# Kernel optimization log

Hardware: AMD Instinct MI355X
Metric: run time of the kernel (lower is better)

The kernel has to match this reference:

```python
import jax, jax.numpy as jnp
import numpy as np

B, S, IN, OUT, SPLIT = 4, 2048, 4096, 4096, 1024


def setup_inputs() -> dict:
    key = jax.random.key(0)
    ks = jax.random.split(key, 14)
    def n(k, shape, scale=1.0):
        return jax.random.normal(k, shape, dtype=jnp.float32) * scale
    return {
        "x": n(ks[0], (B, S, IN)),
        "V": n(ks[1], (SPLIT, IN)),
        "U": n(ks[2], (OUT, SPLIT)),
        "v2": n(ks[3], (1, IN), 0.05),
        "v1": n(ks[4], (1, SPLIT), 0.05),
        "u2": n(ks[5], (1, SPLIT), 0.05),
        "u1": n(ks[6], (1, OUT), 0.05),
        "V_R": n(ks[7], (SPLIT, IN)),
        "U_R": n(ks[8], (OUT, SPLIT)),
        "v2_R": n(ks[9], (1, IN), 0.05),
        "v1_R": n(ks[10], (1, SPLIT), 0.05),
        "u2_R": n(ks[11], (1, SPLIT), 0.05),
        "u1_R": n(ks[12], (1, OUT), 0.05),
        "bias": n(ks[13], (OUT,), 0.02),
    }


def _quantize(w):
    # ITQ binarization: sign(w) with straight-through estimator semantics
    return w + jax.lax.stop_gradient(jnp.sign(w) - w)


def _compute_forward(x2d, V, U, v2, v1, u2, u1):
    # x2d: [T, in]; V: [split, in]; U: [out, split]
    Vq = _quantize(V)
    Uq = _quantize(U)
    v1u2 = v1 * u2  # [1, split]
    h = (x2d * v2) @ Vq.T          # [T, split]
    return (h * v1u2) @ Uq.T * u1  # [T, out]


def reference(x, V, U, v2, v1, u2, u1, V_R, U_R, v2_R, v1_R, u2_R, u1_R, bias):
    lead = x.shape[:-1]
    x2d = x.reshape(-1, x.shape[-1])
    y = _compute_forward(x2d, V, U, v2, v1, u2, u1)
    y = y + _compute_forward(x2d, V_R, U_R, v2_R, v1_R, u2_R, u1_R)
    y = y + bias
    return y.reshape(lead + (U.shape[0],))
```

## Files before the change

### kernel.cpp

```cpp
#include <hip/hip_runtime.h>


typedef __bf16 bf16x8 __attribute__((ext_vector_type(8)));
typedef float floatx4 __attribute__((ext_vector_type(4)));

__device__ __forceinline__ unsigned short f2bf_rne(float f) {
    union { float f; unsigned u; } v; v.f = f;
    unsigned r = v.u + 0x7FFFu + ((v.u >> 16) & 1u);
    return (unsigned short)(r >> 16);
}

__device__ __forceinline__ float sgnf(float w) {
    return (float)((w > 0.f) - (w < 0.f));
}

__device__ __forceinline__ void async_copy16(const void* g, void* l) {
    __builtin_amdgcn_global_load_lds(
        (const __attribute__((address_space(1))) void*)g,
        (__attribute__((address_space(3))) void*)l, 16, 0, 0);
}

#define FENCE() asm volatile("" ::: "memory")
#define BAR() do { FENCE(); __builtin_amdgcn_s_barrier(); FENCE(); } while (0)
#define VMW(N) asm volatile("s_waitcnt vmcnt(" #N ")" ::: "memory")
#define LGKM(N) asm volatile("s_waitcnt lgkmcnt(" #N ")" ::: "memory")


__global__ void prep_all_kernel(const float* __restrict__ x,
                                unsigned short* __restrict__ xb,
                                const float* __restrict__ V, const float* __restrict__ V_R,
                                const float* __restrict__ v2, const float* __restrict__ v2_R,
                                const float* __restrict__ U, const float* __restrict__ U_R,
                                const float* __restrict__ v1, const float* __restrict__ v1_R,
                                const float* __restrict__ u2, const float* __restrict__ u2_R,
                                const float* __restrict__ u1, const float* __restrict__ u1_R,
                                unsigned short* __restrict__ W1,
                                unsigned short* __restrict__ W2) {
    int bid = blockIdx.x;
    if (bid < 32768) {
        int i = bid * blockDim.x + threadIdx.x;
        float4 v = ((const float4*)x)[i];
        ushort4 o;
        o.x = f2bf_rne(v.x); o.y = f2bf_rne(v.y);
        o.z = f2bf_rne(v.z); o.w = f2bf_rne(v.w);
        ((ushort4*)xb)[i] = o;
    } else if (bid < 40960) {
        int i = (bid - 32768) * blockDim.x + threadIdx.x;
        int idx = i << 2;
        int scat = idx >> 12;
        int k = idx & 4095;
        const float* Vp; const float* sp;
        if (scat < 1024) { Vp = V + ((size_t)scat << 12); sp = v2; }
        else             { Vp = V_R + ((size_t)(scat - 1024) << 12); sp = v2_R; }
        float4 w = *(const float4*)(Vp + k);
        float4 s = *(const float4*)(sp + k);
        ushort4 o;
        o.x = f2bf_rne(sgnf(w.x) * s.x);
        o.y = f2bf_rne(sgnf(w.y) * s.y);
        o.z = f2bf_rne(sgnf(w.z) * s.z);
        o.w = f2bf_rne(sgnf(w.w) * s.w);
        ((ushort4*)W1)[i] = o;
    } else {
        int i = (bid - 40960) * blockDim.x + threadIdx.x;
        int idx = i << 2;
        int o = idx >> 11;
        int scat = idx & 2047;
        int branch = scat >> 10;
        int s = scat & 1023;
        const float* Up  = branch ? U_R  : U;
        const float* v1p = branch ? v1_R : v1;
        const float* u2p = branch ? u2_R : u2;
        float u1v = (branch ? u1_R : u1)[o];
        float4 w = *(const float4*)(Up + ((size_t)o << 10) + s);
        float4 a = *(const float4*)(v1p + s);
        float4 b = *(const float4*)(u2p + s);
        ushort4 out;
        out.x = f2bf_rne(sgnf(w.x) * a.x * b.x * u1v);
        out.y = f2bf_rne(sgnf(w.y) * a.y * b.y * u1v);
        out.z = f2bf_rne(sgnf(w.z) * a.z * b.z * u1v);
        out.w = f2bf_rne(sgnf(w.w) * a.w * b.w * u1v);
        ((ushort4*)W2)[i] = out;
    }
}


template <bool OUT_BF16, bool ADD_BIAS>
__global__ __launch_bounds__(512, 2)
void gemm256(const unsigned short* __restrict__ A,
             const unsigned short* __restrict__ B,
             void* __restrict__ Cv,
             const float* __restrict__ bias,
             int M, int N, int K, int ntn) {
    (void)M;
    __shared__ __align__(16) unsigned short As[2][2][128 * 64];
    __shared__ __align__(16) unsigned short Bs[2][2][128 * 64];

    const int tid = threadIdx.x;
    const int lane = tid & 63;
    const int wave = tid >> 6;
    const int warp_m = wave >> 2;
    const int warp_n = wave & 3;

    const int nwg = gridDim.x;
    const int hw = blockIdx.x;
    const int swz = (hw & 7) * (nwg >> 3) + (hw >> 3);
    const int tm = swz / ntn;
    const int tn = swz - tm * ntn;
    const int m0 = tm << 8;
    const int n0 = tn << 8;

    const int srow = tid >> 3;
    const int scg8 = (((tid & 7) ^ (srow & 7)) << 3);
    const int ldst = tid << 3;
    const size_t Ks = (size_t)K;

    auto stA = [&](int buf, int mh, int kt) {
        const unsigned short* g = A + (size_t)(m0 + (mh << 6) + srow) * Ks + (kt << 6) + scg8;
        async_copy16(g,             &As[buf][mh][ldst]);
        async_copy16(g + (Ks << 7), &As[buf][mh][4096 + ldst]);
    };
    auto stB = [&](int buf, int nh, int kt) {
        const unsigned short* g = B + (size_t)(n0 + ((srow >> 5) << 6) + (nh << 5) + (srow & 31)) * Ks
                                    + (kt << 6) + scg8;
        async_copy16(g,             &Bs[buf][nh][ldst]);
        async_copy16(g + (Ks << 7), &Bs[buf][nh][4096 + ldst]);
    };

    const int fm = lane & 15;
    const int cgl = lane >> 4;
    const int key = fm & 7;
    const int ok0 = ((cgl ^ key) << 3);
    const int ok1 = (((4 | cgl) ^ key) << 3);

    auto lda = [&](bf16x8 (&dst)[4][2], int buf, int mh) {
        const unsigned short* base = &As[buf][mh][0];
#pragma unroll
        for (int mi = 0; mi < 4; ++mi) {
            const unsigned short* p = base + (((warp_m << 6) + (mi << 4) + fm) << 6);
            dst[mi][0] = *(const bf16x8*)(p + ok0);
            dst[mi][1] = *(const bf16x8*)(p + ok1);
        }
    };
    auto ldb = [&](bf16x8 (&dst)[2][2], int buf, int nh) {
        const unsigned short* base = &Bs[buf][nh][0];
#pragma unroll
        for (int ni = 0; ni < 2; ++ni) {
            const unsigned short* p = base + (((warp_n << 5) + (ni << 4) + fm) << 6);
            dst[ni][0] = *(const bf16x8*)(p + ok0);
            dst[ni][1] = *(const bf16x8*)(p + ok1);
        }
    };

    floatx4 acc[8][4];
#pragma unroll
    for (int i = 0; i < 8; ++i)
#pragma unroll
        for (int j = 0; j < 4; ++j)
#pragma unroll
            for (int r = 0; r < 4; ++r) acc[i][j][r] = 0.f;

    bf16x8 a0[4][2], a1[4][2], b0[2][2], b1[2][2];

#define MMAQ(aS, bS, MH, NH) do { \
    __builtin_amdgcn_s_setprio(1); \
    _Pragma("unroll") \
    for (int mi_ = 0; mi_ < 4; ++mi_) { \
      _Pragma("unroll") \
      for (int ni_ = 0; ni_ < 2; ++ni_) { \
        acc[(MH)*4 + mi_][(NH)*2 + ni_] = __builtin_amdgcn_mfma_f32_16x16x32_bf16( \
            aS[mi_][0], bS[ni_][0], acc[(MH)*4 + mi_][(NH)*2 + ni_], 0, 0, 0); \
        acc[(MH)*4 + mi_][(NH)*2 + ni_] = __builtin_amdgcn_mfma_f32_16x16x32_bf16( \
            aS[mi_][1], bS[ni_][1], acc[(MH)*4 + mi_][(NH)*2 + ni_], 0, 0, 0); \
      } } \
    __builtin_amdgcn_s_setprio(0); \
  } while (0)

    stB(0, 0, 0); stA(0, 0, 0); stB(0, 1, 0); stA(0, 1, 0);
    stB(1, 0, 1); stA(1, 0, 1); stB(1, 1, 1);
    VMW(6);
    BAR();

    const int NT = K >> 6;
    for (int i = 0; i < (NT >> 1) - 1; ++i) {
        const int ok = 2 * i + 1, fk = 2 * i + 2, gk = 2 * i + 3;
        lda(a0, 0, 0); ldb(b0, 0, 0);
        stA(1, 1, ok);
        LGKM(8);
        BAR(); LGKM(0);
        MMAQ(a0, b0, 0, 0);
        BAR();
        ldb(b1, 0, 1);
        stB(0, 0, fk);
        BAR(); LGKM(0);
        MMAQ(a0, b1, 0, 1);
        BAR();
        lda(a1, 0, 1);
        stA(0, 0, fk);
        BAR(); LGKM(0);
        MMAQ(a1, b1, 1, 1);
        BAR();
        stB(0, 1, fk);
        MMAQ(a1, b0, 1, 0);
        VMW(6);
        BAR();
        lda(a0, 1, 0); ldb(b0, 1, 0);
        stA(0, 1, fk);
        LGKM(8);
        BAR(); LGKM(0);
        MMAQ(a0, b0, 0, 0);
        BAR();
        ldb(b1, 1, 1);
        stB(1, 0, gk);
        BAR(); LGKM(0);
        MMAQ(a0, b1, 0, 1);
        BAR();
        lda(a1, 1, 1);
        stA(1, 0, gk);
        BAR(); LGKM(0);
        MMAQ(a1, b1, 1, 1);
        BAR();
        stB(1, 1, gk);
        MMAQ(a1, b0, 1, 0);
        VMW(6);
        BAR();
    }
    {
        lda(a0, 0, 0); ldb(b0, 0, 0);
        stA(1, 1, NT - 1);
        LGKM(8);
        BAR(); LGKM(0);
        MMAQ(a0, b0, 0, 0);
        BAR();
        ldb(b1, 0, 1);
        BAR(); LGKM(0);
        MMAQ(a0, b1, 0, 1);
        BAR();
        lda(a1, 0, 1);
        BAR(); LGKM(0);
        MMAQ(a1, b1, 1, 1);
        BAR();
        MMAQ(a1, b0, 1, 0);
        VMW(0);
        BAR();
        lda(a0, 1, 0); ldb(b0, 1, 0);
        ldb(b1, 1, 1); lda(a1, 1, 1);
        MMAQ(a0, b0, 0, 0);
        MMAQ(a0, b1, 0, 1);
        MMAQ(a1, b1, 1, 1);
        MMAQ(a1, b0, 1, 0);
    }
#undef MMAQ

    const int rq = (lane >> 4) << 2;
    const int col = lane & 15;
#pragma unroll
    for (int mi = 0; mi < 8; ++mi) {
#pragma unroll
        for (int r = 0; r < 4; ++r) {
            const int gm = m0 + (warp_m << 7) + (mi << 4) + rq + r;
            const size_t base = (size_t)gm * (size_t)N;
#pragma unroll
            for (int ni = 0; ni < 4; ++ni) {
                const int gn = n0 + (warp_n << 6) + (ni << 4) + col;
                float v = acc[mi][ni][r];
                if (ADD_BIAS) v += bias[gn];
                if (OUT_BF16)
                    ((unsigned short*)Cv)[base + gn] = f2bf_rne(v);
                else
                    ((float*)Cv)[base + gn] = v;
            }
        }
    }
}


extern "C" void kernel_launch(void* const* d_in, const int* in_sizes, int n_in,
                              void* d_out, int out_size, void* d_ws, size_t ws_size,
                              hipStream_t stream) {
    const float* x    = (const float*)d_in[0];
    const float* V    = (const float*)d_in[1];
    const float* U    = (const float*)d_in[2];
    const float* v2   = (const float*)d_in[3];
    const float* v1   = (const float*)d_in[4];
    const float* u2   = (const float*)d_in[5];
    const float* u1   = (const float*)d_in[6];
    const float* V_R  = (const float*)d_in[7];
    const float* U_R  = (const float*)d_in[8];
    const float* v2_R = (const float*)d_in[9];
    const float* v1_R = (const float*)d_in[10];
    const float* u2_R = (const float*)d_in[11];
    const float* u1_R = (const float*)d_in[12];
    const float* bias = (const float*)d_in[13];
    float* out = (float*)d_out;

    char* ws = (char*)d_ws;
    unsigned short* Xb = (unsigned short*)ws;
    unsigned short* W1 = (unsigned short*)(ws + (size_t)67108864);
    unsigned short* W2 = (unsigned short*)(ws + (size_t)67108864 + 16777216);
    unsigned short* H  = (unsigned short*)(ws + (size_t)67108864 + 33554432);

    prep_all_kernel<<<49152, 256, 0, stream>>>(x, Xb, V, V_R, v2, v2_R,
                                               U, U_R, v1, v1_R, u2, u2_R, u1, u1_R,
                                               W1, W2);

    gemm256<true, false><<<dim3(256), 512, 0, stream>>>(Xb, W1, (void*)H, nullptr,
                                                        8192, 2048, 4096, 8);
    gemm256<false, true><<<dim3(512), 512, 0, stream>>>(H, W2, (void*)out, bias,
                                                        8192, 4096, 2048, 16);
}
```

Before: 532.8 us.

## Software-pipeline LDS fragment loads against MFMA by double-buffering B fragments

After: 982.2 us. 84.3% more time.

```diff
diff --git a/kernel.cpp b/kernel.cpp
--- a/kernel.cpp
+++ b/kernel.cpp
@@ -159,7 +159,7 @@
 #pragma unroll
             for (int r = 0; r < 4; ++r) acc[i][j][r] = 0.f;
 
-    bf16x8 a0[4][2], a1[4][2], b0[2][2], b1[2][2];
+    bf16x8 a0[4][2], a1[4][2], b0A[2][2], b0B[2][2], b1[2][2];
 
 #define MMAQ(aS, bS, MH, NH) do { \
     __builtin_amdgcn_s_setprio(1); \
@@ -179,75 +179,88 @@
     stB(1, 0, 1); stA(1, 0, 1); stB(1, 1, 1);
     VMW(6);
     BAR();
+    lda(a0, 0, 0); ldb(b0A, 0, 0);
 
     const int NT = K >> 6;
     for (int i = 0; i < (NT >> 1) - 1; ++i) {
-        const int ok = 2 * i + 1, fk = 2 * i + 2, gk = 2 * i + 3;
-        lda(a0, 0, 0); ldb(b0, 0, 0);
-        stA(1, 1, ok);
+        const int okt = 2 * i + 1, fk = 2 * i + 2, gk = 2 * i + 3;
+        stA(1, 1, okt);
+        BAR();
+        ldb(b1, 0, 1);
+        LGKM(4);
+        MMAQ(a0, b0A, 0, 0);
+        BAR();
+        stB(0, 0, fk);
+        BAR();
+        lda(a1, 0, 1);
         LGKM(8);
-        BAR(); LGKM(0);
-        MMAQ(a0, b0, 0, 0);
-        BAR();
-        ldb(b1, 0, 1);
-        stB(0, 0, fk);
-        BAR(); LGKM(0);
         MMAQ(a0, b1, 0, 1);
         BAR();
-        lda(a1, 0, 1);
         stA(0, 0, fk);
-        BAR(); LGKM(0);
+        VMW(4);
+        BAR();
+        ldb(b0B, 1, 0);
+        LGKM(4);
         MMAQ(a1, b1, 1, 1);
         BAR();
         stB(0, 1, fk);
-        MMAQ(a1, b0, 1, 0);
-        VMW(6);
-        BAR();
-        lda(a0, 1, 0); ldb(b0, 1, 0);
+        BAR();
+        lda(a0, 1, 0);
+        MMAQ(a1, b0A, 1, 0);
+        BAR();
         stA(0, 1, fk);
+        BAR();
+        ldb(b1, 1, 1);
+        LGKM(4);
+        MMAQ(a0, b0B, 0, 0);
+        BAR();
+        stB(1, 0, gk);
+        BAR();
+        lda(a1, 1, 1);
         LGKM(8);
-        BAR(); LGKM(0);
-        MMAQ(a0, b0, 0, 0);
-        BAR();
-        ldb(b1, 1, 1);
-        stB(1, 0, gk);
-        BAR(); LGKM(0);
         MMAQ(a0, b1, 0, 1);
         BAR();
-        lda(a1, 1, 1);
         stA(1, 0, gk);
-        BAR(); LGKM(0);
+        VMW(4);
+        BAR();
+        ldb(b0A, 0, 0);
+        LGKM(4);
         MMAQ(a1, b1, 1, 1);
         BAR();
         stB(1, 1, gk);
-        MMAQ(a1, b0, 1, 0);
-        VMW(6);
+        BAR();
+        lda(a0, 0, 0);
+        MMAQ(a1, b0B, 1, 0);
         BAR();
     }
     {
-        lda(a0, 0, 0); ldb(b0, 0, 0);
         stA(1, 1, NT - 1);
+        BAR();
+        ldb(b1, 0, 1);
+        LGKM(4);
+        MMAQ(a0, b0A, 0, 0);
+        BAR();
+        lda(a1, 0, 1);
         LGKM(8);
-        BAR(); LGKM(0);
-        MMAQ(a0, b0, 0, 0);
-        BAR();
-        ldb(b1, 0, 1);
-        BAR(); LGKM(0);
         MMAQ(a0, b1, 0, 1);
         BAR();
-        lda(a1, 0, 1);
-        BAR(); LGKM(0);
+        VMW(0);
+        BAR();
+        ldb(b0B, 1, 0);
+        LGKM(4);
         MMAQ(a1, b1, 1, 1);
         BAR();
-        MMAQ(a1, b0, 1, 0);
-        VMW(0);
-        BAR();
-        lda(a0, 1, 0); ldb(b0, 1, 0);
-        ldb(b1, 1, 1); lda(a1, 1, 1);
-        MMAQ(a0, b0, 0, 0);
+        lda(a0, 1, 0);
+        MMAQ(a1, b0A, 1, 0);
+        ldb(b1, 1, 1);
+        LGKM(4);
+        MMAQ(a0, b0B, 0, 0);
+        lda(a1, 1, 1);
+        LGKM(8);
         MMAQ(a0, b1, 0, 1);
+        LGKM(0);
         MMAQ(a1, b1, 1, 1);
-        MMAQ(a1, b0, 1, 0);
+        MMAQ(a1, b0B, 1, 0);
     }
 #undef MMAQ
 
```
